# Kernel tuning notes

Hardware: AMD Instinct MI355X
Metric: run time of the kernel (lower is better)

Reference implementation:

```python
import jax, jax.numpy as jnp
import numpy as np

B, S, D, H = 2, 2048, 1024, 16
DK = D // H

def setup_inputs() -> dict:
    key = jax.random.key(0)
    ks = jax.random.split(key, 12)
    s = 1.0 / np.sqrt(D)
    return {
        "q": jax.random.normal(ks[0], (B, S, D), jnp.float32),
        "k": jax.random.normal(ks[1], (B, S, D), jnp.float32),
        "v": jax.random.normal(ks[2], (B, S, D), jnp.float32),
        "mask": jnp.ones((1, 1, S, S), jnp.int32),
        "Wq": jax.random.normal(ks[3], (D, D), jnp.float32) * s,
        "bq": jnp.zeros((D,), jnp.float32),
        "Wk": jax.random.normal(ks[4], (D, D), jnp.float32) * s,
        "bk": jnp.zeros((D,), jnp.float32),
        "Wv": jax.random.normal(ks[5], (D, D), jnp.float32) * s,
        "bv": jnp.zeros((D,), jnp.float32),
        "Wo": jax.random.normal(ks[6], (D, D), jnp.float32) * s,
        "bo": jnp.zeros((D,), jnp.float32),
    }

def reference(q, k, v, mask, Wq, bq, Wk, bk, Wv, bv, Wo, bo):
    # projections (torch Linear: x @ W^T + b)
    Q = q @ Wq.T + bq
    K = k @ Wk.T + bk
    V = v @ Wv.T + bv
    # split heads: [B,S,D] -> [B,H,S,DK]
    def split(x):
        return x.reshape(B, S, H, DK).transpose(0, 2, 1, 3)
    Qh, Kh, Vh = split(Q), split(K), split(V)
    scores = jnp.einsum('bhqd,bhkd->bhqk', Qh, Kh) / jnp.sqrt(jnp.float32(DK))
    scores = jnp.where(mask == 0, jnp.float32(-1e9), scores)
    attn = jax.nn.softmax(scores, axis=-1)  # dropout p=0.0 -> identity
    x = jnp.einsum('bhqk,bhkd->bhqd', attn, Vh)
    x = x.transpose(0, 2, 1, 3).reshape(B, S, D)
    return x @ Wo.T + bo
```

## Files before the change

### kernel.cpp

```cpp
#include <hip/hip_runtime.h>
#include <hip/hip_bf16.h>
#include <stdint.h>

#define B_    2
#define S_    2048
#define D_    1024
#define H_    16
#define NTOK  (B_ * S_)

typedef __attribute__((ext_vector_type(8))) short bf16x8;
typedef __attribute__((ext_vector_type(4))) float f32x4;
typedef __attribute__((ext_vector_type(16))) float f32x16;
typedef __attribute__((ext_vector_type(2))) float float2v;
typedef __attribute__((ext_vector_type(2))) __bf16 bfv2;

static __device__ __forceinline__ unsigned short f2bf(float f) {
    unsigned int u = __float_as_uint(f);
    unsigned int r = (u + 0x7FFFu + ((u >> 16) & 1u)) >> 16;
    return (unsigned short)r;
}
static __device__ __forceinline__ unsigned int pkbf(float a, float b) {
    float2v fv = {a, b};
    bfv2 r = __builtin_convertvector(fv, bfv2);
    unsigned int u;
    __builtin_memcpy(&u, &r, 4);
    return u;
}

using g_cu32 = __attribute__((address_space(1))) const unsigned int;
using l_u32  = __attribute__((address_space(3))) unsigned int;
static __device__ __forceinline__ void gld16(const void* g, void* l) {
    __builtin_amdgcn_global_load_lds((g_cu32*)g, (l_u32*)l, 16, 0, 0);
}

#define QN ((size_t)NTOK * D_)
#define WN ((size_t)D_ * D_)

__global__ __launch_bounds__(256) void prep_kernel(
    const float* __restrict__ q, const float* __restrict__ k, const float* __restrict__ v,
    const float* __restrict__ Wq, const float* __restrict__ Wk,
    const float* __restrict__ Wv, const float* __restrict__ Wo,
    const int* __restrict__ mask,
    unsigned short* __restrict__ qb, unsigned short* __restrict__ kb,
    unsigned short* __restrict__ vb, unsigned short* __restrict__ wqb,
    unsigned short* __restrict__ wkb, unsigned short* __restrict__ wvb,
    unsigned short* __restrict__ wob, int* __restrict__ flags) {
    __shared__ int anyz;
    if (blockIdx.x < 8192) {
        size_t i = ((size_t)blockIdx.x * 256 + threadIdx.x) * 8;
        const float* s; unsigned short* d; size_t off;
        if (i < QN)          { s = q; d = qb; off = i; }
        else if (i < 2 * QN) { s = k; d = kb; off = i - QN; }
        else if (i < 3 * QN) { s = v; d = vb; off = i - 2 * QN; }
        else {
            size_t j = i - 3 * QN;
            int wi = (int)(j >> 20);
            s = (wi == 0) ? Wq : (wi == 1) ? Wk : (wi == 2) ? Wv : Wo;
            d = (wi == 0) ? wqb : (wi == 1) ? wkb : (wi == 2) ? wvb : wob;
            off = j & (WN - 1);
        }
        float4 a = *(const float4*)(s + off);
        float4 b = *(const float4*)(s + off + 4);
        uint4 pk;
        pk.x = pkbf(a.x, a.y); pk.y = pkbf(a.z, a.w);
        pk.z = pkbf(b.x, b.y); pk.w = pkbf(b.z, b.w);
        *(uint4*)(d + off) = pk;
    } else {
        if (threadIdx.x == 0) anyz = 0;
        __syncthreads();
        int bid2 = blockIdx.x - 8192;
        const int qt = bid2 >> 5, kt = bid2 & 31;
        int az = 0;
        for (int i = threadIdx.x; i < 64 * 64; i += 256) {
            int r = i >> 6, c = i & 63;
            az |= (mask[(size_t)(qt * 64 + r) * S_ + kt * 64 + c] == 0) ? 1 : 0;
        }
        if (az) atomicOr(&anyz, 1);
        __syncthreads();
        if (threadIdx.x == 0) flags[qt * 32 + kt] = anyz;
    }
}

struct GemmArgs {
    const unsigned short* A[3];
    const unsigned short* W[3];
    const float* bias[3];
    void* C[3];
    int mode[3];
    float scale[3];
};

template<int BMT>
__global__ __launch_bounds__(256, 3) void gemm_async(GemmArgs ga) {
    constexpr int MI   = BMT / 64;
    constexpr int AREG = BMT / 16;
    constexpr int APW  = AREG / 4;
    const int z = blockIdx.z;
    const unsigned short* __restrict__ A = ga.A[z];
    const unsigned short* __restrict__ W = ga.W[z];
    const float* __restrict__ bias = ga.bias[z];
    void* C = ga.C[z];
    const int mode = ga.mode[z];
    const float scl = ga.scale[z];

    __shared__ unsigned short As[AREG * 512];
    __shared__ unsigned short Ws[8 * 512];

    const int t    = threadIdx.x;
    const int lane = t & 63;
    const int w    = t >> 6;
    const int ln31 = lane & 31;
    const int lh   = lane >> 5;
    const int wrow = w >> 1, wcol = w & 1;
    const int m0 = blockIdx.x * BMT, n0 = blockIdx.y * 128;

    const unsigned short* gA[APW]; unsigned short* lA[APW];
#pragma unroll
    for (int i = 0; i < APW; ++i) {
        int r = w * APW + i, rg = r >> 1, ks = r & 1;
        gA[i] = A + (size_t)(m0 + rg * 32 + ln31) * D_ + ks * 16 + lh * 8;
        lA[i] = &As[r * 512];
    }
    const unsigned short* gW[2]; unsigned short* lW[2];
#pragma unroll
    for (int i = 0; i < 2; ++i) {
        int r = w * 2 + i, rg = r >> 1, ks = r & 1;
        gW[i] = W + (size_t)(n0 + rg * 32 + ln31) * D_ + ks * 16 + lh * 8;
        lW[i] = &Ws[r * 512];
    }

    f32x16 acc[MI][2];
#pragma unroll
    for (int i = 0; i < MI; ++i)
#pragma unroll
        for (int j = 0; j < 2; ++j) acc[i][j] = (f32x16)0.0f;

    for (int k0 = 0; k0 < D_ / 32; ++k0) {
#pragma unroll
        for (int i = 0; i < APW; ++i) { gld16(gA[i], lA[i]); gA[i] += 32; }
#pragma unroll
        for (int i = 0; i < 2; ++i) { gld16(gW[i], lW[i]); gW[i] += 32; }
        __syncthreads();

#pragma unroll
        for (int ks = 0; ks < 2; ++ks) {
            bf16x8 af[MI], bw[2];
#pragma unroll
            for (int mi = 0; mi < MI; ++mi)
                af[mi] = *(const bf16x8*)&As[((wrow * MI + mi) * 2 + ks) * 512 + lane * 8];
#pragma unroll
            for (int ni = 0; ni < 2; ++ni)
                bw[ni] = *(const bf16x8*)&Ws[((wcol * 2 + ni) * 2 + ks) * 512 + lane * 8];
#pragma unroll
            for (int mi = 0; mi < MI; ++mi)
#pragma unroll
                for (int ni = 0; ni < 2; ++ni)
                    acc[mi][ni] = __builtin_amdgcn_mfma_f32_32x32x16_bf16(
                        af[mi], bw[ni], acc[mi][ni], 0, 0, 0);
        }
        __syncthreads();
    }

#pragma unroll
    for (int ni = 0; ni < 2; ++ni) {
        int col = n0 + wcol * 64 + ni * 32 + ln31;
        float bv = bias[col];
#pragma unroll
        for (int mi = 0; mi < MI; ++mi) {
            int rbase = m0 + wrow * (BMT / 2) + mi * 32 + 4 * lh;
            if (mode == 0) {
                float* Co = (float*)C;
#pragma unroll
                for (int rg = 0; rg < 4; ++rg)
#pragma unroll
                    for (int rr = 0; rr < 4; ++rr) {
                        int row = rbase + 8 * rg + rr;
                        Co[(size_t)row * D_ + col] = (acc[mi][ni][rg * 4 + rr] + bv) * scl;
                    }
            } else if (mode == 1) {
                unsigned short* Co = (unsigned short*)C;
#pragma unroll
                for (int rg = 0; rg < 4; ++rg)
#pragma unroll
                    for (int rr = 0; rr < 4; ++rr) {
                        int row = rbase + 8 * rg + rr;
                        Co[(size_t)row * D_ + col] = f2bf((acc[mi][ni][rg * 4 + rr] + bv) * scl);
                    }
            } else {
                unsigned short* Co = (unsigned short*)C;
                int hh = col >> 6, d = col & 63;
#pragma unroll
                for (int rg = 0; rg < 4; ++rg) {
                    int tok = rbase + 8 * rg;
                    int bb = tok >> 11, sb = tok & (S_ - 1);
                    uint2 pk;
                    pk.x = pkbf((acc[mi][ni][rg * 4 + 0] + bv) * scl,
                                (acc[mi][ni][rg * 4 + 1] + bv) * scl);
                    pk.y = pkbf((acc[mi][ni][rg * 4 + 2] + bv) * scl,
                                (acc[mi][ni][rg * 4 + 3] + bv) * scl);
                    *(uint2*)(Co + ((size_t)((bb * H_ + hh) * 64 + d)) * S_ + sb) = pk;
                }
            }
        }
    }
}

__global__ __launch_bounds__(256, 2) void flash5(
    const unsigned short* __restrict__ Qb, const unsigned short* __restrict__ Kb,
    const unsigned short* __restrict__ Vtg, const int* __restrict__ mask,
    const int* __restrict__ flags, unsigned short* __restrict__ Xb) {
    __shared__ unsigned short Ks[2][4096];
    __shared__ unsigned short Vs[2][4096];
    __shared__ unsigned short Ps[8192];

    const int t    = threadIdx.x;
    const int lane = t & 63;
    const int w    = t >> 6;
    const int fr   = lane & 15;
    const int kq   = lane >> 4;
    const int qt = blockIdx.x, hd = blockIdx.y, b = blockIdx.z;
    const int q0 = qt * 128;
    const int qw = q0 + w * 32;
    const int swz = fr & 7;

    bf16x8 qf[2][2];
#pragma unroll
    for (int g = 0; g < 2; ++g) {
        const unsigned short* qp = Qb + (size_t)(b * S_ + qw + g * 16 + fr) * D_ + hd * 64;
        qf[g][0] = *(const bf16x8*)(qp + kq * 8);
        qf[g][1] = *(const bf16x8*)(qp + 32 + kq * 8);
    }

    int fl = (lane < 32) ? flags[(qw >> 6) * 32 + lane] : 0;
    unsigned int fmask = (unsigned int)__ballot(fl != 0);

    const unsigned short* kbase =
        Kb + (size_t)(b * S_ + w * 16 + fr) * D_ + hd * 64 + kq * 8;
    const unsigned short* vbase =
        Vtg + ((size_t)((b * H_ + hd) * 64 + w * 16 + fr)) * S_ + kq * 8;

#pragma unroll
    for (int j = 0; j < 2; ++j) {
        gld16(kbase + j * 32, (char*)&Ks[0][0] + w * 2048 + j * 1024);
        gld16(vbase + j * 32, (char*)&Vs[0][0] + w * 2048 + j * 1024);
    }

    f32x4 o[2][4];
#pragma unroll
    for (int g = 0; g < 2; ++g)
#pragma unroll
        for (int i = 0; i < 4; ++i) o[g][i] = (f32x4)0.0f;
    float l_i[2] = {0.0f, 0.0f};

    for (int kt = 0; kt < 32; ++kt) {
        const int cur = kt & 1;
        __syncthreads();
        if (kt < 31) {
#pragma unroll
            for (int j = 0; j < 2; ++j) {
                gld16(kbase + (size_t)(kt + 1) * 64 * D_ + j * 32,
                      (char*)&Ks[cur ^ 1][0] + w * 2048 + j * 1024);
                gld16(vbase + (size_t)(kt + 1) * 64 + j * 32,
                      (char*)&Vs[cur ^ 1][0] + w * 2048 + j * 1024);
            }
        }

        f32x4 st[2][4];
#pragma unroll
        for (int g = 0; g < 2; ++g)
#pragma unroll
            for (int mi = 0; mi < 4; ++mi) st[g][mi] = (f32x4)0.0f;
#pragma unroll
        for (int kk = 0; kk < 2; ++kk)
#pragma unroll
            for (int mi = 0; mi < 4; ++mi) {
                bf16x8 a = *(const bf16x8*)&Ks[cur][mi * 1024 + ((kk * 4 + kq) * 16 + fr) * 8];
                st[0][mi] = __builtin_amdgcn_mfma_f32_16x16x32_bf16(a, qf[0][kk], st[0][mi], 0, 0, 0);
                st[1][mi] = __builtin_amdgcn_mfma_f32_16x16x32_bf16(a, qf[1][kk], st[1][mi], 0, 0, 0);
            }

        if ((fmask >> kt) & 1u) {
#pragma unroll
            for (int g = 0; g < 2; ++g)
#pragma unroll
                for (int mi = 0; mi < 4; ++mi) {
                    int4 mv = *(const int4*)&mask[(size_t)(qw + g * 16 + fr) * S_ + kt * 64 + mi * 16 + kq * 4];
                    if (mv.x == 0) st[g][mi][0] = -3e8f;
                    if (mv.y == 0) st[g][mi][1] = -3e8f;
                    if (mv.z == 0) st[g][mi][2] = -3e8f;
                    if (mv.w == 0) st[g][mi][3] = -3e8f;
                }
        }

#pragma unroll
        for (int g = 0; g < 2; ++g)
#pragma unroll
            for (int mi = 0; mi < 4; ++mi) {
                float e0 = exp2f(st[g][mi][0]), e1 = exp2f(st[g][mi][1]);
                float e2 = exp2f(st[g][mi][2]), e3 = exp2f(st[g][mi][3]);
                l_i[g] += (e0 + e1) + (e2 + e3);
                uint2 pk;
                pk.x = pkbf(e0, e1);
                pk.y = pkbf(e2, e3);
                int chunk = mi * 2 + (kq >> 1);
                *(uint2*)&Ps[(w * 32 + g * 16 + fr) * 64 + ((chunk ^ swz) << 3) + ((kq & 1) << 2)] = pk;
            }

#pragma unroll
        for (int kk = 0; kk < 2; ++kk) {
            int c = kk * 4 + kq;
            bf16x8 pb0 = *(const bf16x8*)&Ps[(w * 32 + fr) * 64 + ((c ^ swz) << 3)];
            bf16x8 pb1 = *(const bf16x8*)&Ps[(w * 32 + 16 + fr) * 64 + ((c ^ swz) << 3)];
#pragma unroll
            for (int mi = 0; mi < 4; ++mi) {
                bf16x8 a = *(const bf16x8*)&Vs[cur][mi * 1024 + ((kk * 4 + kq) * 16 + fr) * 8];
                o[0][mi] = __builtin_amdgcn_mfma_f32_16x16x32_bf16(a, pb0, o[0][mi], 0, 0, 0);
                o[1][mi] = __builtin_amdgcn_mfma_f32_16x16x32_bf16(a, pb1, o[1][mi], 0, 0, 0);
            }
        }
    }

#pragma unroll
    for (int g = 0; g < 2; ++g) {
        float lg = l_i[g];
        lg += __shfl_xor(lg, 16, 64);
        lg += __shfl_xor(lg, 32, 64);
        float rl = 1.0f / lg;
#pragma unroll
        for (int mi = 0; mi < 4; ++mi) {
            uint2 pk;
            pk.x = pkbf(o[g][mi][0] * rl, o[g][mi][1] * rl);
            pk.y = pkbf(o[g][mi][2] * rl, o[g][mi][3] * rl);
            *(uint2*)(Xb + (size_t)(b * S_ + qw + g * 16 + fr) * D_ + hd * 64 + mi * 16 + kq * 4) = pk;
        }
    }
}

extern "C" void kernel_launch(void* const* d_in, const int* in_sizes, int n_in,
                              void* d_out, int out_size, void* d_ws, size_t ws_size,
                              hipStream_t stream) {
    const float* q    = (const float*)d_in[0];
    const float* k    = (const float*)d_in[1];
    const float* v    = (const float*)d_in[2];
    const int*   mask = (const int*)d_in[3];
    const float* Wq   = (const float*)d_in[4];
    const float* bq   = (const float*)d_in[5];
    const float* Wk   = (const float*)d_in[6];
    const float* bk   = (const float*)d_in[7];
    const float* Wv   = (const float*)d_in[8];
    const float* bv   = (const float*)d_in[9];
    const float* Wo   = (const float*)d_in[10];
    const float* bo   = (const float*)d_in[11];
    float* out = (float*)d_out;

    unsigned short* qb  = (unsigned short*)d_ws;
    unsigned short* kb  = qb + QN;
    unsigned short* vb  = kb + QN;
    unsigned short* Qf  = vb + QN;
    unsigned short* Kf  = Qf + QN;
    unsigned short* Vt  = Kf + QN;
    unsigned short* wqb = Vt + QN;
    unsigned short* wkb = wqb + WN;
    unsigned short* wvb = wkb + WN;
    unsigned short* wob = wvb + WN;
    int* flags = (int*)(wob + WN);

    const float SC = 0.18033688011112042f;

    prep_kernel<<<9216, 256, 0, stream>>>(q, k, v, Wq, Wk, Wv, Wo, mask,
                                          qb, kb, vb, wqb, wkb, wvb, wob, flags);

    GemmArgs g1;
    g1.A[0] = qb;  g1.W[0] = wqb; g1.bias[0] = bq; g1.C[0] = Qf; g1.mode[0] = 1; g1.scale[0] = SC;
    g1.A[1] = kb;  g1.W[1] = wkb; g1.bias[1] = bk; g1.C[1] = Kf; g1.mode[1] = 1; g1.scale[1] = 1.0f;
    g1.A[2] = vb;  g1.W[2] = wvb; g1.bias[2] = bv; g1.C[2] = Vt; g1.mode[2] = 2; g1.scale[2] = 1.0f;
    gemm_async<128><<<dim3(NTOK / 128, D_ / 128, 3), 256, 0, stream>>>(g1);

    flash5<<<dim3(S_ / 128, H_, B_), 256, 0, stream>>>(Qf, Kf, Vt, mask, flags, Qf);

    GemmArgs g2;
    g2.A[0] = Qf; g2.W[0] = wob; g2.bias[0] = bo; g2.C[0] = out; g2.mode[0] = 0; g2.scale[0] = 1.0f;
    g2.A[1] = g2.A[2] = nullptr; g2.W[1] = g2.W[2] = nullptr;
    g2.bias[1] = g2.bias[2] = nullptr; g2.C[1] = g2.C[2] = nullptr;
    g2.mode[1] = g2.mode[2] = 0; g2.scale[1] = g2.scale[2] = 1.0f;
    gemm_async<64><<<dim3(NTOK / 64, D_ / 128, 1), 256, 0, stream>>>(g2);
}
```

Before: 278.3 us.

## Double-buffer LDS tiles in projection GEMM to overlap loads with MFMA

The GEMM kernel gets two shared-memory buffers for the A and W tiles. The async global-to-LDS load of the next K-slice is issued right after the barrier, so it overlaps the MFMA work on the current slice. This also removes the second per-iteration barrier, leaving one sync per step. In exchange LDS use doubles, which may limit how many blocks fit per CU.

```diff
diff --git a/kernel.cpp b/kernel.cpp
--- a/kernel.cpp
+++ b/kernel.cpp
@@ -103,8 +103,8 @@
     const int mode = ga.mode[z];
     const float scl = ga.scale[z];
 
-    __shared__ unsigned short As[AREG * 512];
-    __shared__ unsigned short Ws[8 * 512];
+    __shared__ unsigned short As[2][AREG * 512];
+    __shared__ unsigned short Ws[2][8 * 512];
 
     const int t    = threadIdx.x;
     const int lane = t & 63;
@@ -114,19 +114,19 @@
     const int wrow = w >> 1, wcol = w & 1;
     const int m0 = blockIdx.x * BMT, n0 = blockIdx.y * 128;
 
-    const unsigned short* gA[APW]; unsigned short* lA[APW];
+    const unsigned short* gA[APW]; int lAoff[APW];
 #pragma unroll
     for (int i = 0; i < APW; ++i) {
         int r = w * APW + i, rg = r >> 1, ks = r & 1;
         gA[i] = A + (size_t)(m0 + rg * 32 + ln31) * D_ + ks * 16 + lh * 8;
-        lA[i] = &As[r * 512];
-    }
-    const unsigned short* gW[2]; unsigned short* lW[2];
+        lAoff[i] = r * 512;
+    }
+    const unsigned short* gW[2]; int lWoff[2];
 #pragma unroll
     for (int i = 0; i < 2; ++i) {
         int r = w * 2 + i, rg = r >> 1, ks = r & 1;
         gW[i] = W + (size_t)(n0 + rg * 32 + ln31) * D_ + ks * 16 + lh * 8;
-        lW[i] = &Ws[r * 512];
+        lWoff[i] = r * 512;
     }
 
     f32x16 acc[MI][2];
@@ -135,22 +135,32 @@
 #pragma unroll
         for (int j = 0; j < 2; ++j) acc[i][j] = (f32x16)0.0f;
 
-    for (int k0 = 0; k0 < D_ / 32; ++k0) {
-#pragma unroll
-        for (int i = 0; i < APW; ++i) { gld16(gA[i], lA[i]); gA[i] += 32; }
-#pragma unroll
-        for (int i = 0; i < 2; ++i) { gld16(gW[i], lW[i]); gW[i] += 32; }
+#pragma unroll
+    for (int i = 0; i < APW; ++i) gld16(gA[i], &As[0][lAoff[i]]);
+#pragma unroll
+    for (int i = 0; i < 2; ++i) gld16(gW[i], &Ws[0][lWoff[i]]);
+
+    constexpr int NIT = D_ / 32;
+    for (int k0 = 0; k0 < NIT; ++k0) {
+        const int cur = k0 & 1;
         __syncthreads();
+        if (k0 + 1 < NIT) {
+            const size_t koff = (size_t)(k0 + 1) * 32;
+#pragma unroll
+            for (int i = 0; i < APW; ++i) gld16(gA[i] + koff, &As[cur ^ 1][lAoff[i]]);
+#pragma unroll
+            for (int i = 0; i < 2; ++i) gld16(gW[i] + koff, &Ws[cur ^ 1][lWoff[i]]);
+        }
 
 #pragma unroll
         for (int ks = 0; ks < 2; ++ks) {
             bf16x8 af[MI], bw[2];
 #pragma unroll
             for (int mi = 0; mi < MI; ++mi)
-                af[mi] = *(const bf16x8*)&As[((wrow * MI + mi) * 2 + ks) * 512 + lane * 8];
+                af[mi] = *(const bf16x8*)&As[cur][((wrow * MI + mi) * 2 + ks) * 512 + lane * 8];
 #pragma unroll
             for (int ni = 0; ni < 2; ++ni)
-                bw[ni] = *(const bf16x8*)&Ws[((wcol * 2 + ni) * 2 + ks) * 512 + lane * 8];
+                bw[ni] = *(const bf16x8*)&Ws[cur][((wcol * 2 + ni) * 2 + ks) * 512 + lane * 8];
 #pragma unroll
             for (int mi = 0; mi < MI; ++mi)
 #pragma unroll
@@ -158,7 +168,6 @@
                     acc[mi][ni] = __builtin_amdgcn_mfma_f32_32x32x16_bf16(
                         af[mi], bw[ni], acc[mi][ni], 0, 0, 0);
         }
-        __syncthreads();
     }
 
 #pragma unroll
```

Result: no change. 277.7 us (-0.2%).
